# Optimization experiments

Hardware: AMD Instinct MI355X
Metric: run time of the kernel (lower is better)

The kernel has to match this reference:

```python
import jax, jax.numpy as jnp
import numpy as np

MARGIN = 0.5

def _pairwise_dist(x):
    # Euclidean cdist with grad-safe sqrt (diagonal is exactly zero).
    sq = jnp.sum(x * x, axis=1)
    d2 = sq[:, None] + sq[None, :] - 2.0 * (x @ x.T)
    d2 = jnp.maximum(d2, 0.0)
    safe = jnp.where(d2 > 0.0, d2, 1.0)
    return jnp.where(d2 > 0.0, jnp.sqrt(safe), 0.0)

def setup_inputs() -> dict:
    key = jax.random.key(0)
    k1, k2 = jax.random.split(key)
    embeddings = jax.random.normal(k1, (8192, 128), dtype=jnp.float32)
    labels = jax.random.randint(k2, (8192,), 0, 256, dtype=jnp.int64)
    return {"embeddings": embeddings, "labels": labels}

def reference(embeddings, labels):
    B = embeddings.shape[0]
    dist = _pairwise_dist(embeddings)                      # [B, B]
    same = labels[:, None] == labels[None, :]              # [B, B]
    eye = jnp.eye(B, dtype=bool)
    pos_mask = same & ~eye
    neg_mask = ~same
    neg_inf = jnp.float32(-jnp.inf)
    pos_inf = jnp.float32(jnp.inf)
    hardest_pos = jnp.max(jnp.where(pos_mask, dist, neg_inf), axis=1)  # [B]
    hardest_neg = jnp.min(jnp.where(neg_mask, dist, pos_inf), axis=1)  # [B]
    valid = jnp.any(pos_mask, axis=1) & jnp.any(neg_mask, axis=1)      # [B]
    per_anchor = jnp.maximum(hardest_pos - hardest_neg + MARGIN, 0.0)
    per_anchor = jnp.where(valid, per_anchor, 0.0)
    num = jnp.sum(valid.astype(jnp.float32))
    return jnp.sum(per_anchor) / jnp.maximum(num, 1.0)
```

## Files before the change

### kernel.cpp

```cpp
#include <hip/hip_runtime.h>
#include <hip/hip_bf16.h>
#include <stdint.h>


typedef __bf16 bf16x8 __attribute__((ext_vector_type(8)));
typedef float f32x4 __attribute__((ext_vector_type(4)));

constexpr int NB = 8192;
constexpr int ND = 128;
constexpr int SPLIT = 32;
constexpr int JR = NB / SPLIT;
constexpr int BN = 64;
constexpr int NT = JR / BN;
constexpr int BM = 256;
constexpr int NRB = NB / BM;

constexpr size_t OFF_XB  = 0;
constexpr size_t OFF_SQ  = (size_t)NB * ND * 2;
constexpr size_t OFF_LAB = OFF_SQ + (size_t)NB * 4;
constexpr size_t OFF_HP  = OFF_LAB + (size_t)NB * 4;
constexpr size_t OFF_HN  = OFF_HP + (size_t)SPLIT * NB * 4;
constexpr size_t OFF_ACC = OFF_HN + (size_t)SPLIT * NB * 4;

__device__ __forceinline__ unsigned short f2bf(float f) {
  union { float f; uint32_t u; } c; c.f = f;
  uint32_t u = c.u;
  u += 0x7fffu + ((u >> 16) & 1u);
  return (unsigned short)(u >> 16);
}

__global__ __launch_bounds__(256) void prep_kernel(
    const float* __restrict__ x, const int* __restrict__ labels,
    unsigned short* __restrict__ xb, float* __restrict__ sq,
    int* __restrict__ lab, float* __restrict__ acc, int* __restrict__ cnt) {
  if (blockIdx.x == 0 && threadIdx.x == 0) {
    acc[0] = 0.f;
    acc[1] = 0.f;
    *cnt = 0;
  }
  const int row = blockIdx.x * 8 + (threadIdx.x >> 5);
  const int sub = threadIdx.x & 31;
  const float4 v = *reinterpret_cast<const float4*>(x + (size_t)row * ND + sub * 4);
  ushort4 o;
  o.x = f2bf(v.x); o.y = f2bf(v.y); o.z = f2bf(v.z); o.w = f2bf(v.w);
  *reinterpret_cast<ushort4*>(xb + (size_t)row * ND + sub * 4) = o;
  float s = v.x * v.x + v.y * v.y + v.z * v.z + v.w * v.w;
#pragma unroll
  for (int m = 1; m < 32; m <<= 1) s += __shfl_xor(s, m);
  if (sub == 0) {
    sq[row] = s;
    lab[row] = labels[row];
  }
}

__global__ __launch_bounds__(256, 2) void hard_kernel(
    const unsigned short* __restrict__ xb, const float* __restrict__ sq,
    const int* __restrict__ lab, float* __restrict__ hp_out,
    float* __restrict__ hn_out) {
  __shared__ __align__(16) char smem[2][BN * ND * 2];
  __shared__ float sqh[JR];
  __shared__ int labl[JR];
  const int tid = threadIdx.x;
  const int lane = tid & 63;
  const int w = tid >> 6;
  const int c16 = lane & 15;
  const int g4 = lane >> 4;
  const int rowbase = blockIdx.x * BM + w * 64;
  const int colbase = blockIdx.y * JR;

  auto stage = [&](int buf, int tile) {
    const char* gbase = reinterpret_cast<const char*>(xb) +
                        ((size_t)(colbase + tile * BN)) * (ND * 2);
#pragma unroll
    for (int rnd = 0; rnd < 4; ++rnd) {
      const int L = rnd * 4096 + tid * 16;
      const int slot = (L >> 4) & 15;
      const int col = L >> 8;
      const int src = (L & ~0xF0) | ((slot ^ (col & 15)) << 4);
      __builtin_amdgcn_global_load_lds(
          (const __attribute__((address_space(1))) unsigned int*)(gbase + src),
          (__attribute__((address_space(3))) unsigned int*)(&smem[buf][L]),
          16, 0, 0);
    }
  };

  stage(0, 0);
  {
    sqh[tid] = -0.5f * sq[colbase + tid];
    labl[tid] = lab[colbase + tid];
  }

  bf16x8 afrag[4][4];
#pragma unroll
  for (int rt = 0; rt < 4; ++rt) {
    const unsigned short* ap =
        xb + ((size_t)(rowbase + rt * 16 + c16)) * ND + g4 * 8;
#pragma unroll
    for (int kk = 0; kk < 4; ++kk)
      afrag[rt][kk] = *reinterpret_cast<const bf16x8*>(ap + kk * 32);
  }
  int labr[4][4];
#pragma unroll
  for (int rt = 0; rt < 4; ++rt)
#pragma unroll
    for (int rr = 0; rr < 4; ++rr)
      labr[rt][rr] = lab[rowbase + rt * 16 + g4 * 4 + rr];

  float hpu[4][4], hnu[4][4];
#pragma unroll
  for (int rt = 0; rt < 4; ++rt)
#pragma unroll
    for (int rr = 0; rr < 4; ++rr) {
      hpu[rt][rr] = __builtin_inff();
      hnu[rt][rr] = -__builtin_inff();
    }

  __syncthreads();

  for (int t = 0; t < NT; ++t) {
    if (t + 1 < NT) stage((t + 1) & 1, t + 1);
    const char* sb = smem[t & 1];
#pragma unroll
    for (int jj = 0; jj < 4; ++jj) {
      const int colL = jj * 16 + c16;
      const int jidx = t * BN + colL;
      const float sqc = sqh[jidx];
      const int labc = labl[jidx];

      bf16x8 bfrag[4];
#pragma unroll
      for (int kk = 0; kk < 4; ++kk) {
        const int kbyte = kk * 64 + g4 * 16;
        const int a = colL * 256 + (kbyte ^ (c16 << 4));
        bfrag[kk] = *reinterpret_cast<const bf16x8*>(sb + a);
      }

      f32x4 acc[4];
#pragma unroll
      for (int rt = 0; rt < 4; ++rt) acc[rt] = (f32x4){sqc, sqc, sqc, sqc};
      __builtin_amdgcn_s_setprio(1);
#pragma unroll
      for (int kk = 0; kk < 4; ++kk)
#pragma unroll
        for (int rt = 0; rt < 4; ++rt)
          acc[rt] = __builtin_amdgcn_mfma_f32_16x16x32_bf16(
              afrag[rt][kk], bfrag[kk], acc[rt], 0, 0, 0);
      __builtin_amdgcn_s_setprio(0);

#pragma unroll
      for (int rt = 0; rt < 4; ++rt)
#pragma unroll
        for (int rr = 0; rr < 4; ++rr) {
          const float u = acc[rt][rr];
          const bool same = (labc == labr[rt][rr]);
          hpu[rt][rr] = fminf(hpu[rt][rr], same ? u : __builtin_inff());
          hnu[rt][rr] = fmaxf(hnu[rt][rr], same ? -__builtin_inff() : u);
        }
    }
    __syncthreads();
  }

#pragma unroll
  for (int rt = 0; rt < 4; ++rt)
#pragma unroll
    for (int rr = 0; rr < 4; ++rr) {
      float p = hpu[rt][rr], n = hnu[rt][rr];
#pragma unroll
      for (int m = 1; m <= 8; m <<= 1) {
        p = fminf(p, __shfl_xor(p, m));
        n = fmaxf(n, __shfl_xor(n, m));
      }
      if (c16 == 0) {
        const int rg = rowbase + rt * 16 + g4 * 4 + rr;
        hp_out[(size_t)blockIdx.y * NB + rg] = p;
        hn_out[(size_t)blockIdx.y * NB + rg] = n;
      }
    }
}

__global__ __launch_bounds__(256) void reduce_kernel(
    const float* __restrict__ hp, const float* __restrict__ hn,
    const float* __restrict__ sq, float* __restrict__ acc,
    int* __restrict__ cnt_done, float* __restrict__ out) {
  const int a = blockIdx.x * 256 + threadIdx.x;
  float p = __builtin_inff(), n = -__builtin_inff();
#pragma unroll 8
  for (int s = 0; s < SPLIT; ++s) {
    p = fminf(p, hp[(size_t)s * NB + a]);
    n = fmaxf(n, hn[(size_t)s * NB + a]);
  }
  const float sqa = sq[a];
  const float d2p = fmaxf(fmaf(-2.f, p, sqa), 0.f);
  const float d2n = fmaxf(fmaf(-2.f, n, sqa), 0.f);
  const bool valid = (d2p > 1.0f) && (n > -1e37f);
  float loss = valid ? fmaxf(sqrtf(d2p) - sqrtf(d2n) + 0.5f, 0.f) : 0.f;
  float c = valid ? 1.f : 0.f;
#pragma unroll
  for (int m = 1; m < 64; m <<= 1) {
    loss += __shfl_xor(loss, m);
    c += __shfl_xor(c, m);
  }
  __shared__ float ls[4], cs[4];
  const int w = threadIdx.x >> 6, lane = threadIdx.x & 63;
  if (lane == 0) { ls[w] = loss; cs[w] = c; }
  __syncthreads();
  if (threadIdx.x == 0) {
    atomicAdd(&acc[0], ls[0] + ls[1] + ls[2] + ls[3]);
    atomicAdd(&acc[1], cs[0] + cs[1] + cs[2] + cs[3]);
    __threadfence();
    const int old = atomicAdd(cnt_done, 1);
    if (old == (NB / 256) - 1) {
      const float l = atomicAdd(&acc[0], 0.0f);
      const float nvalid = atomicAdd(&acc[1], 0.0f);
      out[0] = l / fmaxf(nvalid, 1.f);
    }
  }
}

extern "C" void kernel_launch(void* const* d_in, const int* in_sizes, int n_in,
                              void* d_out, int out_size, void* d_ws,
                              size_t ws_size, hipStream_t stream) {
  const float* x = (const float*)d_in[0];
  const int* labels = (const int*)d_in[1];
  char* ws = (char*)d_ws;
  unsigned short* xb = (unsigned short*)(ws + OFF_XB);
  float* sq = (float*)(ws + OFF_SQ);
  int* lab = (int*)(ws + OFF_LAB);
  float* hp = (float*)(ws + OFF_HP);
  float* hn = (float*)(ws + OFF_HN);
  float* acc = (float*)(ws + OFF_ACC);
  int* cnt = (int*)(ws + OFF_ACC + 8);

  prep_kernel<<<NB / 8, 256, 0, stream>>>(x, labels, xb, sq, lab, acc, cnt);
  hard_kernel<<<dim3(NRB, SPLIT), 256, 0, stream>>>(xb, sq, lab, hp, hn);
  reduce_kernel<<<NB / 256, 256, 0, stream>>>(hp, hn, sq, acc, cnt,
                                              (float*)d_out);
}
```

Baseline: 94.29 us.

## Fuse final reduction into hard kernel via per-panel tickets, retile for occupancy

Removes the separate reduce kernel: each row panel counts finished column splits with an atomic ticket, and the last block for a panel reduces that panel's partial min/max and adds its loss into a global accumulator. Tiles are reshaped (BM 256→128, SPLIT 32→16, 32 rows per wave), launch bounds are raised to 4 blocks per CU, and setprio is dropped. This saves one launch and improves occupancy, but the tail work moves onto the last blocks and each wave gets less MFMA reuse per B fragment.

```diff
diff --git a/kernel.cpp b/kernel.cpp
--- a/kernel.cpp
+++ b/kernel.cpp
@@ -8,11 +8,11 @@
 
 constexpr int NB = 8192;
 constexpr int ND = 128;
-constexpr int SPLIT = 32;
+constexpr int SPLIT = 16;
 constexpr int JR = NB / SPLIT;
 constexpr int BN = 64;
 constexpr int NT = JR / BN;
-constexpr int BM = 256;
+constexpr int BM = 128;
 constexpr int NRB = NB / BM;
 
 constexpr size_t OFF_XB  = 0;
@@ -32,11 +32,9 @@
 __global__ __launch_bounds__(256) void prep_kernel(
     const float* __restrict__ x, const int* __restrict__ labels,
     unsigned short* __restrict__ xb, float* __restrict__ sq,
-    int* __restrict__ lab, float* __restrict__ acc, int* __restrict__ cnt) {
-  if (blockIdx.x == 0 && threadIdx.x == 0) {
-    acc[0] = 0.f;
-    acc[1] = 0.f;
-    *cnt = 0;
+    int* __restrict__ lab, int* __restrict__ ctrl ) {
+  if (blockIdx.x == 0 && threadIdx.x < 3 + NRB) {
+    ctrl[threadIdx.x] = 0;
   }
   const int row = blockIdx.x * 8 + (threadIdx.x >> 5);
   const int sub = threadIdx.x & 31;
@@ -53,20 +51,27 @@
   }
 }
 
-__global__ __launch_bounds__(256, 2) void hard_kernel(
+__global__ __launch_bounds__(256, 4) void hard_kernel(
     const unsigned short* __restrict__ xb, const float* __restrict__ sq,
     const int* __restrict__ lab, float* __restrict__ hp_out,
-    float* __restrict__ hn_out) {
+    float* __restrict__ hn_out, int* __restrict__ ctrl,
+    float* __restrict__ out) {
   __shared__ __align__(16) char smem[2][BN * ND * 2];
   __shared__ float sqh[JR];
   __shared__ int labl[JR];
+  __shared__ int lastflag;
+  __shared__ float ls[4], cs[4];
   const int tid = threadIdx.x;
   const int lane = tid & 63;
   const int w = tid >> 6;
   const int c16 = lane & 15;
   const int g4 = lane >> 4;
-  const int rowbase = blockIdx.x * BM + w * 64;
+  const int panel = blockIdx.x;
+  const int rowbase = panel * BM + w * 32;
   const int colbase = blockIdx.y * JR;
+  float* accf = reinterpret_cast<float*>(ctrl);
+  int* gcnt = ctrl + 2;
+  int* pcnt = ctrl + 3;
 
   auto stage = [&](int buf, int tile) {
     const char* gbase = reinterpret_cast<const char*>(xb) +
@@ -86,29 +91,33 @@
 
   stage(0, 0);
   {
-    sqh[tid] = -0.5f * sq[colbase + tid];
-    labl[tid] = lab[colbase + tid];
-  }
-
-  bf16x8 afrag[4][4];
-#pragma unroll
-  for (int rt = 0; rt < 4; ++rt) {
+    const int i2 = tid * 2;
+    const float2 s2 = *reinterpret_cast<const float2*>(&sq[colbase + i2]);
+    sqh[i2] = -0.5f * s2.x;
+    sqh[i2 + 1] = -0.5f * s2.y;
+    *reinterpret_cast<int2*>(&labl[i2]) =
+        *reinterpret_cast<const int2*>(&lab[colbase + i2]);
+  }
+
+  bf16x8 afrag[2][4];
+#pragma unroll
+  for (int rt = 0; rt < 2; ++rt) {
     const unsigned short* ap =
         xb + ((size_t)(rowbase + rt * 16 + c16)) * ND + g4 * 8;
 #pragma unroll
     for (int kk = 0; kk < 4; ++kk)
       afrag[rt][kk] = *reinterpret_cast<const bf16x8*>(ap + kk * 32);
   }
-  int labr[4][4];
-#pragma unroll
-  for (int rt = 0; rt < 4; ++rt)
+  int labr[2][4];
+#pragma unroll
+  for (int rt = 0; rt < 2; ++rt)
 #pragma unroll
     for (int rr = 0; rr < 4; ++rr)
       labr[rt][rr] = lab[rowbase + rt * 16 + g4 * 4 + rr];
 
-  float hpu[4][4], hnu[4][4];
-#pragma unroll
-  for (int rt = 0; rt < 4; ++rt)
+  float hpu[2][4], hnu[2][4];
+#pragma unroll
+  for (int rt = 0; rt < 2; ++rt)
 #pragma unroll
     for (int rr = 0; rr < 4; ++rr) {
       hpu[rt][rr] = __builtin_inff();
@@ -135,20 +144,18 @@
         bfrag[kk] = *reinterpret_cast<const bf16x8*>(sb + a);
       }
 
-      f32x4 acc[4];
-#pragma unroll
-      for (int rt = 0; rt < 4; ++rt) acc[rt] = (f32x4){sqc, sqc, sqc, sqc};
-      __builtin_amdgcn_s_setprio(1);
+      f32x4 acc[2];
+#pragma unroll
+      for (int rt = 0; rt < 2; ++rt) acc[rt] = (f32x4){sqc, sqc, sqc, sqc};
 #pragma unroll
       for (int kk = 0; kk < 4; ++kk)
 #pragma unroll
-        for (int rt = 0; rt < 4; ++rt)
+        for (int rt = 0; rt < 2; ++rt)
           acc[rt] = __builtin_amdgcn_mfma_f32_16x16x32_bf16(
               afrag[rt][kk], bfrag[kk], acc[rt], 0, 0, 0);
-      __builtin_amdgcn_s_setprio(0);
-
-#pragma unroll
-      for (int rt = 0; rt < 4; ++rt)
+
+#pragma unroll
+      for (int rt = 0; rt < 2; ++rt)
 #pragma unroll
         for (int rr = 0; rr < 4; ++rr) {
           const float u = acc[rt][rr];
@@ -161,7 +168,7 @@
   }
 
 #pragma unroll
-  for (int rt = 0; rt < 4; ++rt)
+  for (int rt = 0; rt < 2; ++rt)
 #pragma unroll
     for (int rr = 0; rr < 4; ++rr) {
       float p = hpu[rt][rr], n = hnu[rt][rr];
@@ -176,42 +183,48 @@
         hn_out[(size_t)blockIdx.y * NB + rg] = n;
       }
     }
-}
-
-__global__ __launch_bounds__(256) void reduce_kernel(
-    const float* __restrict__ hp, const float* __restrict__ hn,
-    const float* __restrict__ sq, float* __restrict__ acc,
-    int* __restrict__ cnt_done, float* __restrict__ out) {
-  const int a = blockIdx.x * 256 + threadIdx.x;
-  float p = __builtin_inff(), n = -__builtin_inff();
-#pragma unroll 8
-  for (int s = 0; s < SPLIT; ++s) {
-    p = fminf(p, hp[(size_t)s * NB + a]);
-    n = fmaxf(n, hn[(size_t)s * NB + a]);
-  }
-  const float sqa = sq[a];
-  const float d2p = fmaxf(fmaf(-2.f, p, sqa), 0.f);
-  const float d2n = fmaxf(fmaf(-2.f, n, sqa), 0.f);
-  const bool valid = (d2p > 1.0f) && (n > -1e37f);
-  float loss = valid ? fmaxf(sqrtf(d2p) - sqrtf(d2n) + 0.5f, 0.f) : 0.f;
-  float c = valid ? 1.f : 0.f;
+
+  __threadfence();
+  __syncthreads();
+  if (tid == 0) {
+    const int ticket = atomicAdd(&pcnt[panel], 1);
+    lastflag = (ticket == SPLIT - 1);
+  }
+  __syncthreads();
+  if (!lastflag) return;
+  __threadfence();
+
+  float loss = 0.f, c = 0.f;
+  if (tid < BM) {
+    const int a = panel * BM + tid;
+    float p = __builtin_inff(), n = -__builtin_inff();
+#pragma unroll
+    for (int s = 0; s < SPLIT; ++s) {
+      p = fminf(p, hp_out[(size_t)s * NB + a]);
+      n = fmaxf(n, hn_out[(size_t)s * NB + a]);
+    }
+    const float sqa = sq[a];
+    const float d2p = fmaxf(fmaf(-2.f, p, sqa), 0.f);
+    const float d2n = fmaxf(fmaf(-2.f, n, sqa), 0.f);
+    const bool valid = (d2p > 1.0f) && (n > -1e37f);
+    loss = valid ? fmaxf(sqrtf(d2p) - sqrtf(d2n) + 0.5f, 0.f) : 0.f;
+    c = valid ? 1.f : 0.f;
+  }
 #pragma unroll
   for (int m = 1; m < 64; m <<= 1) {
     loss += __shfl_xor(loss, m);
     c += __shfl_xor(c, m);
   }
-  __shared__ float ls[4], cs[4];
-  const int w = threadIdx.x >> 6, lane = threadIdx.x & 63;
   if (lane == 0) { ls[w] = loss; cs[w] = c; }
   __syncthreads();
-  if (threadIdx.x == 0) {
-    atomicAdd(&acc[0], ls[0] + ls[1] + ls[2] + ls[3]);
-    atomicAdd(&acc[1], cs[0] + cs[1] + cs[2] + cs[3]);
+  if (tid == 0) {
+    atomicAdd(&accf[0], ls[0] + ls[1] + ls[2] + ls[3]);
+    atomicAdd(&accf[1], cs[0] + cs[1] + cs[2] + cs[3]);
     __threadfence();
-    const int old = atomicAdd(cnt_done, 1);
-    if (old == (NB / 256) - 1) {
-      const float l = atomicAdd(&acc[0], 0.0f);
-      const float nvalid = atomicAdd(&acc[1], 0.0f);
+    const int old = atomicAdd(gcnt, 1);
+    if (old == NRB - 1) {
+      const float l = atomicAdd(&accf[0], 0.0f);
+      const float nvalid = atomicAdd(&accf[1], 0.0f);
       out[0] = l / fmaxf(nvalid, 1.f);
     }
   }
@@ -228,11 +241,9 @@
   int* lab = (int*)(ws + OFF_LAB);
   float* hp = (float*)(ws + OFF_HP);
   float* hn = (float*)(ws + OFF_HN);
-  float* acc = (float*)(ws + OFF_ACC);
-  int* cnt = (int*)(ws + OFF_ACC + 8);
-
-  prep_kernel<<<NB / 8, 256, 0, stream>>>(x, labels, xb, sq, lab, acc, cnt);
-  hard_kernel<<<dim3(NRB, SPLIT), 256, 0, stream>>>(xb, sq, lab, hp, hn);
-  reduce_kernel<<<NB / 256, 256, 0, stream>>>(hp, hn, sq, acc, cnt,
-                                              (float*)d_out);
-}
+  int* ctrl = (int*)(ws + OFF_ACC);
+
+  prep_kernel<<<NB / 8, 256, 0, stream>>>(x, labels, xb, sq, lab, ctrl);
+  hard_kernel<<<dim3(NRB, SPLIT), 256, 0, stream>>>(xb, sq, lab, hp, hn, ctrl,
+                                                    (float*)d_out);
+}
```

Measured after the change: 175.5 us. 1.86x slower.
